# Kernel tuning notes

Measured on AMD Instinct MI355X. Metric: run time of the kernel, lower is better.

The kernel has to match this reference:

```python
import jax, jax.numpy as jnp
import numpy as np

BITS = 4
IN_F = 4096
OUT_F = 4096
NUMVALS = 200000
TOPX = 10
B, S = 4, 2048


def setup_inputs() -> dict:
    key = jax.random.key(0)
    ks = jax.random.split(key, 9)
    x = jax.random.normal(ks[0], (B, S, IN_F), dtype=jnp.float32)
    qweight = jax.random.randint(ks[1], (IN_F // 32 * BITS, OUT_F),
                                 jnp.iinfo(jnp.int32).min, jnp.iinfo(jnp.int32).max,
                                 dtype=jnp.int32)
    lookup_table = jax.random.normal(ks[2], (OUT_F, 2 ** BITS), dtype=jnp.float32) * 0.02
    bias = jax.random.normal(ks[3], (OUT_F,), dtype=jnp.float32) * 0.01
    rows = jnp.sort(jax.random.randint(ks[4], (OUT_F + 1,), 0, NUMVALS, dtype=jnp.int32))
    rows = rows.at[0].set(0).at[-1].set(NUMVALS)  # valid CSR row pointers
    cols = jax.random.randint(ks[5], (NUMVALS,), 0, IN_F, dtype=jnp.int32)
    vals = jax.random.normal(ks[6], (NUMVALS,), dtype=jnp.float32) * 0.02
    full_rows = jax.random.normal(ks[7], (IN_F, TOPX), dtype=jnp.float32) * 0.02
    full_row_indices = (jnp.arange(TOPX, dtype=jnp.int32) * (OUT_F // TOPX))
    return {"x": x, "qweight": qweight, "lookup_table": lookup_table, "bias": bias,
            "rows": rows, "cols": cols, "vals": vals,
            "full_rows": full_rows, "full_row_indices": full_row_indices}


def _dequant(qweight, lookup_table):
    # unpack 4-bit codes packed along infeatures into each int32 word
    per_word = 32 // BITS
    shifts = (jnp.arange(per_word, dtype=jnp.int32) * BITS)
    codes = (qweight[:, None, :] >> shifts[None, :, None]) & ((1 << BITS) - 1)
    codes = codes.reshape(-1, qweight.shape[1])  # (IN_F, OUT_F)
    # per-output-channel LUT gather: W[i, j] = lut[j, codes[i, j]]
    return jnp.take_along_axis(lookup_table.T, codes, axis=0)  # (IN_F, OUT_F)


def reference(x, qweight, lookup_table, bias, rows, cols, vals, full_rows, full_row_indices):
    w = _dequant(qweight, lookup_table)  # (IN_F, OUT_F) float32
    # CSR sparse outlier correction (row pointers over output channels)
    nnz = vals.shape[0]
    row_ids = jnp.searchsorted(rows, jnp.arange(nnz, dtype=jnp.int32), side="right") - 1
    w = w.at[cols, row_ids].add(vals)
    # topX dense outlier channels
    w = w.at[:, full_row_indices].add(full_rows)
    tokens = x.reshape(-1, x.shape[-1])  # (B*S, IN_F)
    y = tokens @ w + bias
    return y.reshape(x.shape[:-1] + (w.shape[1],))
```

## Files before the change

kernel.cpp:

```cpp
#include <hip/hip_runtime.h>
#include <hip/hip_bf16.h>
#include <stdint.h>

#define IN_F 4096
#define OUT_F 4096
#define MTOK 8192
#define TOPX_N 10
#define NUMVALS 200000

typedef __bf16 bf16x8 __attribute__((ext_vector_type(8)));
typedef float f32x4 __attribute__((ext_vector_type(4)));

__device__ __forceinline__ void gld_lds16(const void* g, void* l) {
    __builtin_amdgcn_global_load_lds((const __attribute__((address_space(1))) void*)g,
                                     (__attribute__((address_space(3))) void*)l, 16, 0, 0);
}

__global__ __launch_bounds__(256) void k_dequant(const int* __restrict__ qw,
                                                 const float* __restrict__ lut,
                                                 __bf16* __restrict__ Wt) {
    __shared__ int qs[64 * 65];
    __shared__ float ls[64 * 16];
    const int b = blockIdx.x;
    const int jc = (b & 63) * 64;
    const int wc = (b >> 6) * 64;
    const int t = threadIdx.x;

    {
        float4 v = *(const float4*)(lut + (size_t)(jc + (t >> 2)) * 16 + (t & 3) * 4);
        *(float4*)(ls + (t >> 2) * 16 + (t & 3) * 4) = v;
    }
#pragma unroll
    for (int p = 0; p < 4; ++p) {
        int idx = t + p * 256;
        int row = idx >> 4;
        int c4 = (idx & 15) * 4;
        int4 v = *(const int4*)(qw + (size_t)(wc + row) * OUT_F + jc + c4);
        int base = row * 65 + c4;
        qs[base] = v.x; qs[base + 1] = v.y; qs[base + 2] = v.z; qs[base + 3] = v.w;
    }
    __syncthreads();

    const int wave = t >> 6, lane = t & 63;
#pragma unroll
    for (int i = 0; i < 16; ++i) {
        const int c = wave * 16 + i;
        const unsigned q = (unsigned)qs[lane * 65 + c];
        const float* lp = ls + c * 16;
        bf16x8 v;
#pragma unroll
        for (int e = 0; e < 8; ++e) v[e] = (__bf16)lp[(q >> (4 * e)) & 15];
        *(bf16x8*)(Wt + (size_t)(jc + c) * IN_F + (size_t)(wc + lane) * 8) = v;
    }
}

__global__ __launch_bounds__(256) void k_csr(const int* __restrict__ rows,
                                             const int* __restrict__ cols,
                                             const float* __restrict__ vals,
                                             __bf16* __restrict__ Wt) {
    int n = blockIdx.x * 256 + threadIdx.x;
    if (n >= NUMVALS) return;
    int lo = 0, hi = OUT_F + 1;
    while (lo < hi) {
        int mid = (lo + hi) >> 1;
        if (rows[mid] <= n) lo = mid + 1; else hi = mid;
    }
    int r = lo - 1;
    int c = cols[n];
    float v = vals[n];
    unsigned* wp = (unsigned*)Wt + (((size_t)r * IN_F + c) >> 1);
    unsigned sh = (c & 1) * 16;
    unsigned old = *wp, assumed;
    do {
        assumed = old;
        union { unsigned u; float f; } cv;
        cv.u = ((assumed >> sh) & 0xFFFFu) << 16;
        __bf16 nb = (__bf16)(cv.f + v);
        unsigned nh = *(unsigned short*)&nb;
        unsigned newv = (assumed & ~(0xFFFFu << sh)) | (nh << sh);
        old = atomicCAS(wp, assumed, newv);
    } while (old != assumed);
}

__global__ void k_topx(const float* __restrict__ fr, const int* __restrict__ fri,
                       __bf16* __restrict__ Wt) {
    int i = blockIdx.x * 256 + threadIdx.x;
    if (i >= IN_F) return;
#pragma unroll
    for (int t = 0; t < TOPX_N; ++t) {
        int j = fri[t];
        __bf16* p = Wt + (size_t)j * IN_F + i;
        *p = (__bf16)((float)*p + fr[(size_t)i * TOPX_N + t]);
    }
}

__global__ void k_cvt(const float* __restrict__ x, __bf16* __restrict__ xb) {
    size_t t = (size_t)blockIdx.x * 256 + threadIdx.x;
    const float4* p = (const float4*)x + 2 * t;
    float4 a = p[0], b = p[1];
    bf16x8 v;
    v[0] = (__bf16)a.x; v[1] = (__bf16)a.y; v[2] = (__bf16)a.z; v[3] = (__bf16)a.w;
    v[4] = (__bf16)b.x; v[5] = (__bf16)b.y; v[6] = (__bf16)b.z; v[7] = (__bf16)b.w;
    ((bf16x8*)xb)[t] = v;
}

__global__ __launch_bounds__(256) void k_gemm(const __bf16* __restrict__ A,
                                              const __bf16* __restrict__ Bt,
                                              const float* __restrict__ bias,
                                              float* __restrict__ C) {
    __shared__ __align__(16) __bf16 As[128 * 32];
    __shared__ __align__(16) __bf16 Bs[128 * 32];
    const int tid = threadIdx.x;
    const int wave = tid >> 6;
    const int lane = tid & 63;
    const int m0 = blockIdx.y * 128;
    const int n0 = blockIdx.x * 128;
    const int wr = (wave >> 1) * 64;
    const int wc = (wave & 1) * 64;
    const int lrow = lane & 15;
    const int lk = lane >> 4;

    const int o0 = wave * 2048 + lane * 16;
    const int o1 = o0 + 1024;
    const int r0 = o0 >> 6, kb0 = o0 & 63;
    const int r1 = o1 >> 6, kb1 = o1 & 63;

    const char* gA0 = (const char*)(A + (size_t)(m0 + r0) * IN_F) + kb0;
    const char* gA1 = (const char*)(A + (size_t)(m0 + r1) * IN_F) + kb1;
    const char* gB0 = (const char*)(Bt + (size_t)(n0 + r0) * IN_F) + kb0;
    const char* gB1 = (const char*)(Bt + (size_t)(n0 + r1) * IN_F) + kb1;
    char* lA0 = (char*)As + o0;
    char* lA1 = (char*)As + o1;
    char* lB0 = (char*)Bs + o0;
    char* lB1 = (char*)Bs + o1;

    f32x4 acc[4][4] = {};

    for (int k0 = 0; k0 < IN_F; k0 += 32) {
        gld_lds16(gA0, lA0);
        gld_lds16(gA1, lA1);
        gld_lds16(gB0, lB0);
        gld_lds16(gB1, lB1);
        gA0 += 64; gA1 += 64; gB0 += 64; gB1 += 64;
        __syncthreads();

        bf16x8 af[4], bf[4];
#pragma unroll
        for (int i = 0; i < 4; ++i)
            af[i] = *(const bf16x8*)(As + (wr + i * 16 + lrow) * 32 + lk * 8);
#pragma unroll
        for (int j = 0; j < 4; ++j)
            bf[j] = *(const bf16x8*)(Bs + (wc + j * 16 + lrow) * 32 + lk * 8);

#pragma unroll
        for (int i = 0; i < 4; ++i)
#pragma unroll
            for (int j = 0; j < 4; ++j)
                acc[i][j] = __builtin_amdgcn_mfma_f32_16x16x32_bf16(af[i], bf[j], acc[i][j], 0, 0, 0);

        __syncthreads();
    }

#pragma unroll
    for (int j = 0; j < 4; ++j) {
        const int col = n0 + wc + j * 16 + lrow;
        const float bj = bias[col];
#pragma unroll
        for (int i = 0; i < 4; ++i) {
            const int mrow = m0 + wr + i * 16 + lk * 4;
#pragma unroll
            for (int r = 0; r < 4; ++r) {
                C[(size_t)(mrow + r) * OUT_F + col] = acc[i][j][r] + bj;
            }
        }
    }
}

extern "C" void kernel_launch(void* const* d_in, const int* in_sizes, int n_in,
                              void* d_out, int out_size, void* d_ws, size_t ws_size,
                              hipStream_t stream) {
    const float* x         = (const float*)d_in[0];
    const int*   qweight   = (const int*)d_in[1];
    const float* lut       = (const float*)d_in[2];
    const float* bias      = (const float*)d_in[3];
    const int*   rows      = (const int*)d_in[4];
    const int*   cols      = (const int*)d_in[5];
    const float* vals      = (const float*)d_in[6];
    const float* full_rows = (const float*)d_in[7];
    const int*   fri       = (const int*)d_in[8];
    float* out = (float*)d_out;

    __bf16* Wt = (__bf16*)d_ws;
    __bf16* xb = (__bf16*)((char*)d_ws + (size_t)OUT_F * IN_F * 2);

    k_dequant<<<dim3(64 * 8), 256, 0, stream>>>(qweight, lut, Wt);
    k_csr<<<dim3((NUMVALS + 255) / 256), 256, 0, stream>>>(rows, cols, vals, Wt);
    k_topx<<<dim3(IN_F / 256), 256, 0, stream>>>(full_rows, fri, Wt);
    k_cvt<<<dim3((size_t)MTOK * IN_F / 8 / 256), 256, 0, stream>>>(x, xb);
    k_gemm<<<dim3(OUT_F / 128, MTOK / 128), 256, 0, stream>>>(xb, Wt, bias, out);
}
```

Baseline: 559.6 us.

## Rewrite GEMM with 256x256 tiles, triple-buffered LDS pipeline and swizzled layout

Replaces the 128x128 single-buffered GEMM with a 512-thread, 256x256-tile kernel. It uses a three-stage global_load_lds ring so loads run ahead of the MFMAs, an XOR-style swizzled LDS layout to avoid bank conflicts, a block-index swizzle for L2 locality, and s_setprio around the MFMA bursts. The aim is to remove the load/compute serialization and the barrier stalls of the old loop, and to raise data reuse per tile. In exchange it uses 96KB of LDS and 128 accumulator floats per thread, which may limit occupancy.

```diff
diff --git a/kernel.cpp b/kernel.cpp
--- a/kernel.cpp
+++ b/kernel.cpp
@@ -104,76 +104,101 @@
     ((bf16x8*)xb)[t] = v;
 }
 
-__global__ __launch_bounds__(256) void k_gemm(const __bf16* __restrict__ A,
-                                              const __bf16* __restrict__ Bt,
-                                              const float* __restrict__ bias,
-                                              float* __restrict__ C) {
-    __shared__ __align__(16) __bf16 As[128 * 32];
-    __shared__ __align__(16) __bf16 Bs[128 * 32];
+#define BK_G 32
+#define NKT (IN_F / BK_G)
+#define TILE_BYTES 16384
+
+__global__ __launch_bounds__(512, 2) void k_gemm(const __bf16* __restrict__ A,
+                                                 const __bf16* __restrict__ Bt,
+                                                 const float* __restrict__ bias,
+                                                 float* __restrict__ C) {
+    __shared__ __align__(1024) char smem[3][2][TILE_BYTES];
+
     const int tid = threadIdx.x;
-    const int wave = tid >> 6;
-    const int lane = tid & 63;
-    const int m0 = blockIdx.y * 128;
-    const int n0 = blockIdx.x * 128;
-    const int wr = (wave >> 1) * 64;
-    const int wc = (wave & 1) * 64;
-    const int lrow = lane & 15;
-    const int lk = lane >> 4;
-
-    const int o0 = wave * 2048 + lane * 16;
-    const int o1 = o0 + 1024;
-    const int r0 = o0 >> 6, kb0 = o0 & 63;
-    const int r1 = o1 >> 6, kb1 = o1 & 63;
-
-    const char* gA0 = (const char*)(A + (size_t)(m0 + r0) * IN_F) + kb0;
-    const char* gA1 = (const char*)(A + (size_t)(m0 + r1) * IN_F) + kb1;
-    const char* gB0 = (const char*)(Bt + (size_t)(n0 + r0) * IN_F) + kb0;
-    const char* gB1 = (const char*)(Bt + (size_t)(n0 + r1) * IN_F) + kb1;
-    char* lA0 = (char*)As + o0;
-    char* lA1 = (char*)As + o1;
-    char* lB0 = (char*)Bs + o0;
-    char* lB1 = (char*)Bs + o1;
-
-    f32x4 acc[4][4] = {};
-
-    for (int k0 = 0; k0 < IN_F; k0 += 32) {
-        gld_lds16(gA0, lA0);
-        gld_lds16(gA1, lA1);
-        gld_lds16(gB0, lB0);
-        gld_lds16(gB1, lB1);
-        gA0 += 64; gA1 += 64; gB0 += 64; gB1 += 64;
-        __syncthreads();
-
-        bf16x8 af[4], bf[4];
-#pragma unroll
-        for (int i = 0; i < 4; ++i)
-            af[i] = *(const bf16x8*)(As + (wr + i * 16 + lrow) * 32 + lk * 8);
-#pragma unroll
-        for (int j = 0; j < 4; ++j)
-            bf[j] = *(const bf16x8*)(Bs + (wc + j * 16 + lrow) * 32 + lk * 8);
-
-#pragma unroll
-        for (int i = 0; i < 4; ++i)
-#pragma unroll
-            for (int j = 0; j < 4; ++j)
-                acc[i][j] = __builtin_amdgcn_mfma_f32_16x16x32_bf16(af[i], bf[j], acc[i][j], 0, 0, 0);
-
-        __syncthreads();
-    }
-
-#pragma unroll
-    for (int j = 0; j < 4; ++j) {
-        const int col = n0 + wc + j * 16 + lrow;
+    const int wave = tid >> 6, lane = tid & 63;
+    const int wm = wave >> 2, wn = wave & 3;
+
+    const int bid = blockIdx.x;
+    const int swz = (bid & 7) * 64 + (bid >> 3);
+    const int n0 = (swz & 15) * 256;
+    const int m0 = (swz >> 4) * 256;
+
+    const int q = lane & 7, g = (lane >> 3) & 3, rh = lane >> 5;
+    const int rloc = ((5 * (q - g + 8)) & 7) + 8 * rh;
+    const int w0 = wave * 2;
+
+    const char* gA0 = (const char*)(A  + (size_t)(m0 + w0 * 16 + rloc) * IN_F) + g * 16;
+    const char* gA1 = gA0 + 16 * IN_F * 2;
+    const char* gB0 = (const char*)(Bt + (size_t)(n0 + w0 * 16 + rloc) * IN_F) + g * 16;
+    const char* gB1 = gB0 + 16 * IN_F * 2;
+    char* lA = (char*)smem[0][0] + w0 * 1024;
+    char* lB = (char*)smem[0][1] + w0 * 1024;
+
+    const int lrow = lane & 15, kk = lane >> 4;
+    const int rdc = ((5 * lrow + kk) & 7) * 16 + kk * 128 + (lrow >> 3) * 512;
+    const int rdA = wm * 8192 + rdc;
+    const int rdB = wn * 4096 + rdc;
+
+#define STAGE(boff, koff) do {                               \
+        gld_lds16(gA0 + (koff), lA + (boff));                \
+        gld_lds16(gA1 + (koff), lA + (boff) + 1024);         \
+        gld_lds16(gB0 + (koff), lB + (boff));                \
+        gld_lds16(gB1 + (koff), lB + (boff) + 1024);         \
+    } while (0)
+
+#define COMPUTE(boff) do {                                                                     \
+        const char* pA = (const char*)smem[0][0] + (boff) + rdA;                               \
+        const char* pB = (const char*)smem[0][1] + (boff) + rdB;                               \
+        bf16x8 bfr[4], af0[4], af1[4];                                                         \
+        _Pragma("unroll") for (int n = 0; n < 4; ++n) bfr[n] = *(const bf16x8*)(pB + n * 1024);\
+        _Pragma("unroll") for (int m = 0; m < 4; ++m) af0[m] = *(const bf16x8*)(pA + m * 1024);\
+        _Pragma("unroll") for (int m = 0; m < 4; ++m) af1[m] = *(const bf16x8*)(pA + 4096 + m * 1024);\
+        __builtin_amdgcn_s_setprio(1);                                                         \
+        _Pragma("unroll") for (int m = 0; m < 4; ++m)                                          \
+            _Pragma("unroll") for (int n = 0; n < 4; ++n)                                      \
+                acc[m][n] = __builtin_amdgcn_mfma_f32_16x16x32_bf16(af0[m], bfr[n], acc[m][n], 0, 0, 0); \
+        _Pragma("unroll") for (int m = 0; m < 4; ++m)                                          \
+            _Pragma("unroll") for (int n = 0; n < 4; ++n)                                      \
+                acc[m + 4][n] = __builtin_amdgcn_mfma_f32_16x16x32_bf16(af1[m], bfr[n], acc[m + 4][n], 0, 0, 0); \
+        __builtin_amdgcn_s_setprio(0);                                                         \
+    } while (0)
+
+    f32x4 acc[8][4] = {};
+
+    STAGE(0, 0);
+    STAGE(32768, 64);
+
+    int cboff = 0, sboff = 65536;
+    for (int t = 0; t < NKT - 1; ++t) {
+        asm volatile("s_waitcnt vmcnt(4)" ::: "memory");
+        __builtin_amdgcn_s_barrier();
+        asm volatile("" ::: "memory");
+        if (t + 2 < NKT) STAGE(sboff, (t + 2) * 64);
+        COMPUTE(cboff);
+        cboff = cboff == 65536 ? 0 : cboff + 32768;
+        sboff = sboff == 65536 ? 0 : sboff + 32768;
+    }
+    asm volatile("s_waitcnt vmcnt(0)" ::: "memory");
+    __builtin_amdgcn_s_barrier();
+    asm volatile("" ::: "memory");
+    COMPUTE(cboff);
+
+    const int m0w = m0 + wm * 128;
+    const int n0w = n0 + wn * 64;
+#pragma unroll
+    for (int n = 0; n < 4; ++n) {
+        const int col = n0w + n * 16 + lrow;
         const float bj = bias[col];
 #pragma unroll
-        for (int i = 0; i < 4; ++i) {
-            const int mrow = m0 + wr + i * 16 + lk * 4;
-#pragma unroll
-            for (int r = 0; r < 4; ++r) {
-                C[(size_t)(mrow + r) * OUT_F + col] = acc[i][j][r] + bj;
-            }
+        for (int m = 0; m < 8; ++m) {
+            const int row = m0w + m * 16 + kk * 4;
+#pragma unroll
+            for (int r = 0; r < 4; ++r)
+                C[(size_t)(row + r) * OUT_F + col] = acc[m][n][r] + bj;
         }
     }
+#undef STAGE
+#undef COMPUTE
 }
 
 extern "C" void kernel_launch(void* const* d_in, const int* in_sizes, int n_in,
@@ -197,5 +222,5 @@
     k_csr<<<dim3((NUMVALS + 255) / 256), 256, 0, stream>>>(rows, cols, vals, Wt);
     k_topx<<<dim3(IN_F / 256), 256, 0, stream>>>(full_rows, fri, Wt);
     k_cvt<<<dim3((size_t)MTOK * IN_F / 8 / 256), 256, 0, stream>>>(x, xb);
-    k_gemm<<<dim3(OUT_F / 128, MTOK / 128), 256, 0, stream>>>(xb, Wt, bias, out);
-}
+    k_gemm<<<dim3((OUT_F / 256) * (MTOK / 256)), 512, 0, stream>>>(xb, Wt, bias, out);
+}
```

Measured after the change: 536.7 us. 1.04x faster.
